# Kernel optimization log

Measured on AMD Instinct MI355X. Metric: run time of the kernel, lower is better.

The kernel has to match this reference:

```python
import jax, jax.numpy as jnp
import numpy as np
from jax import lax

B, T, I, H, O, L = 32, 1024, 128, 512, 128, 2


def _lstm_layer(x, Wih, Whh, bih, bhh):
    # x: [B, T, in]; Wih: [4H, in]; Whh: [4H, H]; PyTorch gate order i,f,g,o
    Hs = Whh.shape[1]
    # Precompute input contribution for all timesteps (one big GEMM)
    xg = jnp.einsum('bti,gi->btg', x, Wih) + bih + bhh  # [B, T, 4H]
    xg_t = jnp.swapaxes(xg, 0, 1)  # [T, B, 4H] for scan

    def step(carry, g_in):
        h, c = carry
        g = g_in + h @ Whh.T  # [B, 4H]
        i, f, gg, o = jnp.split(g, 4, axis=-1)
        i = jax.nn.sigmoid(i)
        f = jax.nn.sigmoid(f)
        gg = jnp.tanh(gg)
        o = jax.nn.sigmoid(o)
        c = f * c + i * gg
        h = o * jnp.tanh(c)
        return (h, c), h

    h0 = jnp.zeros((x.shape[0], Hs), dtype=x.dtype)
    c0 = jnp.zeros((x.shape[0], Hs), dtype=x.dtype)
    (_, _), hs = lax.scan(step, (h0, c0), xg_t)
    return jnp.swapaxes(hs, 0, 1)  # [B, T, H]


def setup_inputs() -> dict:
    key = jax.random.key(0)
    ks = jax.random.split(key, 16)
    s = 1.0 / np.sqrt(H)  # torch LSTM/Linear init scale
    u = lambda k, shape: jax.random.uniform(k, shape, jnp.float32, -s, s)
    return {
        'x': jax.random.normal(ks[0], (B, T, I), jnp.float32),
        'W_ih0': u(ks[1], (4 * H, I)), 'W_hh0': u(ks[2], (4 * H, H)),
        'b_ih0': u(ks[3], (4 * H,)), 'b_hh0': u(ks[4], (4 * H,)),
        'W_ih1': u(ks[5], (4 * H, H)), 'W_hh1': u(ks[6], (4 * H, H)),
        'b_ih1': u(ks[7], (4 * H,)), 'b_hh1': u(ks[8], (4 * H,)),
        'fcW': u(ks[9], (O, H)), 'fcb': u(ks[10], (O,)),
        'fc2W': jax.random.uniform(ks[11], (O, O), jnp.float32, -1.0 / np.sqrt(O), 1.0 / np.sqrt(O)),
        'fc2b': jax.random.uniform(ks[12], (O,), jnp.float32, -1.0 / np.sqrt(O), 1.0 / np.sqrt(O)),
    }


def reference(x, W_ih0, W_hh0, b_ih0, b_hh0, W_ih1, W_hh1, b_ih1, b_hh1, fcW, fcb, fc2W, fc2b):
    h1 = _lstm_layer(x, W_ih0, W_hh0, b_ih0, b_hh0)   # [B, T, H]
    h2 = _lstm_layer(h1, W_ih1, W_hh1, b_ih1, b_hh1)  # [B, T, H]
    out = h2 @ fcW.T + fcb    # [B, T, O]
    out2 = out @ fc2W.T + fc2b  # [B, T, O]
    return out2
```

## Files before the change

### kernel.cpp

```cpp
#include <hip/hip_runtime.h>
#include <math.h>

typedef _Float16 f16;
typedef _Float16 f16x8 __attribute__((ext_vector_type(8)));
typedef _Float16 f16x4 __attribute__((ext_vector_type(4)));
typedef _Float16 f16x2 __attribute__((ext_vector_type(2)));
typedef float f32x16 __attribute__((ext_vector_type(16)));
typedef int i32x4 __attribute__((ext_vector_type(4)));

#define B_ 32
#define T_ 1024
#define I_ 128
#define H_ 512

#define NWG 64
#define THR 512

#define OFF_FLAGS 0UL
#define OFF_H1S   4096UL
#define OFF_H2S   33591296UL
#define OFF_XT    67178496UL

__device__ inline f32x16 mfma32(f16x8 a, f16x8 b, f32x16 c) {
  return __builtin_amdgcn_mfma_f32_32x32x16_f16(a, b, c, 0, 0, 0);
}
__device__ inline float fast_sig(float x) { return 1.f / (1.f + __expf(-x)); }
__device__ inline float fast_tanh(float x) {
  float e = __expf(-2.f * fabsf(x));
  float t = (1.f - e) / (1.f + e);
  return x < 0.f ? -t : t;
}

__device__ inline unsigned ld_sc1_u32(const unsigned* p) {
  unsigned r;
  asm volatile("global_load_dword %0, %1, off sc1\n\ts_waitcnt vmcnt(0)"
               : "=v"(r) : "v"(p) : "memory");
  return r;
}
__device__ inline void st_sc1_u32(unsigned* p, unsigned v) {
  asm volatile("global_store_dword %0, %1, off sc1" :: "v"(p), "v"(v) : "memory");
}

__device__ inline int swz_h(int b, int kbyte) { return b * 1024 + (kbyte ^ ((b & 7) << 4)); }
__device__ inline int swz_x(int b, int kbyte) { return b * 256  + (kbyte ^ ((b & 7) << 4)); }

__global__ __launch_bounds__(256) void prep_xT(const float* __restrict__ x, f16* __restrict__ xT) {
  const int idx = blockIdx.x * 256 + threadIdx.x;
  const int n4 = B_ * T_ * I_ / 4;
  if (idx < n4) {
    const int i4 = idx * 4;
    const int i  = i4 & (I_ - 1);
    const int tt = (i4 >> 7) & (T_ - 1);
    const int b  = i4 >> 17;
    float4 v = *(const float4*)(x + i4);
    f16x4 o;
    o[0] = (f16)v.x; o[1] = (f16)v.y; o[2] = (f16)v.z; o[3] = (f16)v.w;
    *(f16x4*)(xT + ((size_t)tt * B_ + b) * I_ + i) = o;
  }
}

__global__ __launch_bounds__(THR, 1) void lstm_persist(
    const float* __restrict__ Wih0, const float* __restrict__ Whh0,
    const float* __restrict__ bih0, const float* __restrict__ bhh0,
    const float* __restrict__ Wih1, const float* __restrict__ Whh1,
    const float* __restrict__ bih1, const float* __restrict__ bhh1,
    char* ws) {
  __shared__ i32x4 h1l4[2048];
  __shared__ i32x4 h2l4[2048];
  __shared__ i32x4 xl4[512];
  __shared__ float gbuf[2 * 32 * 68];
  __shared__ float biasl[64];

  const int tid  = threadIdx.x;
  const int wgid = blockIdx.x;
  const int role = wgid >> 5;
  const int gid  = wgid & 31;
  const int lane = tid & 63;
  const int wv   = tid >> 6;
  const int nt   = wv & 1;
  const int kq   = (wv >> 1) & 1;
  const int bl   = lane & 31;
  const int kg   = lane >> 5;

  unsigned* flags0 = (unsigned*)(ws + OFF_FLAGS);
  unsigned* flags1 = (unsigned*)(ws + OFF_FLAGS + 2048);
  const char* h1base = ws + OFF_H1S;
  const char* h2base = ws + OFF_H2S;

  if (tid < 64) {
    const int g = tid >> 4, hc = tid & 15;
    const int row = g * 512 + gid * 16 + hc;
    biasl[tid] = role ? (bih1[row] + bhh1[row]) : (bih0[row] + bhh0[row]);
  }

  const int n    = nt * 32 + bl;
  const int wrow = (n >> 4) * 512 + gid * 16 + (n & 15);
  f16x8 wreg[32];
  if (role == 0) {
    if (wv < 4) {
#pragma unroll
      for (int ks = 0; ks < 20; ++ks) {
        const int k = kq * 320 + ks * 16 + kg * 8;
        const float* src = (k < I_) ? (Wih0 + (size_t)wrow * I_ + k)
                                    : (Whh0 + (size_t)wrow * H_ + (k - I_));
        float4 v0 = *(const float4*)(src);
        float4 v1 = *(const float4*)(src + 4);
        f16x8 h;
        h[0] = (f16)v0.x; h[1] = (f16)v0.y; h[2] = (f16)v0.z; h[3] = (f16)v0.w;
        h[4] = (f16)v1.x; h[5] = (f16)v1.y; h[6] = (f16)v1.z; h[7] = (f16)v1.w;
        wreg[ks] = h;
      }
    }
  } else {
    if (wv < 4) {
#pragma unroll
      for (int ks = 0; ks < 32; ++ks) {
        const int k = kq * 512 + ks * 16 + kg * 8;
        const float* src = (k < H_) ? (Wih1 + (size_t)wrow * H_ + k)
                                    : (Whh1 + (size_t)wrow * H_ + (k - H_));
        float4 v0 = *(const float4*)(src);
        float4 v1 = *(const float4*)(src + 4);
        f16x8 h;
        h[0] = (f16)v0.x; h[1] = (f16)v0.y; h[2] = (f16)v0.z; h[3] = (f16)v0.w;
        h[4] = (f16)v1.x; h[5] = (f16)v1.y; h[6] = (f16)v1.z; h[7] = (f16)v1.w;
        wreg[ks] = h;
      }
    }
  }

  float cst0 = 0.f, cst1 = 0.f;
  const char* h1c = (const char*)h1l4;
  const char* h2c = (const char*)h2l4;
  const char* xc  = (const char*)xl4;

  __syncthreads();

  if (role == 0) {
    for (int s = 0; s < T_; ++s) {
      i32x4 xv = ((const i32x4*)(ws + OFF_XT))[(size_t)s * 512 + tid];

      if (s >= 1) {
        if (tid < 64) {
          const unsigned tgt = (unsigned)s;
          const unsigned* fp = flags0 + (tid < 32 ? tid : 0) * 16;
          const bool active = tid < 32;
          for (;;) {
            unsigned v = ld_sc1_u32(fp);
            if (!active) v = tgt;
            if (__all((int)(v >= tgt))) break;
            __builtin_amdgcn_s_sleep(1);
          }
        }
        __syncthreads();
      }

      {
        const i32x4* src = (const i32x4*)(h1base + (size_t)s * 32768);
#pragma unroll
        for (int r = 0; r < 4; ++r) {
          const int u = r * 512 + tid;
          i32x4 v = src[u];
          const int wgs = u >> 6, b = (u >> 1) & 31, half = u & 1;
          *(i32x4*)((char*)h1l4 + swz_h(b, wgs * 32 + half * 16)) = v;
        }
      }
      *(i32x4*)((char*)xl4 + swz_x(tid >> 4, (tid & 15) * 16)) = xv;
      __syncthreads();

      if (wv < 4) {
        f32x16 acc = {};
        if (kq == 0) {
#pragma unroll
          for (int ks = 0; ks < 8; ++ks) {
            f16x8 a = *(const f16x8*)(xc + swz_x(bl, (ks * 16 + kg * 8) * 2));
            acc = mfma32(a, wreg[ks], acc);
          }
#pragma unroll
          for (int ks = 8; ks < 20; ++ks) {
            f16x8 a = *(const f16x8*)(h1c + swz_h(bl, (ks * 16 + kg * 8 - I_) * 2));
            acc = mfma32(a, wreg[ks], acc);
          }
        } else {
#pragma unroll
          for (int ks = 0; ks < 20; ++ks) {
            f16x8 a = *(const f16x8*)(h1c + swz_h(bl, (192 + ks * 16 + kg * 8) * 2));
            acc = mfma32(a, wreg[ks], acc);
          }
        }
        const int cb = nt * 32 + bl;
#pragma unroll
        for (int r = 0; r < 16; ++r) {
          const int row = (r & 3) + 8 * (r >> 2) + 4 * kg;
          gbuf[kq * 2176 + row * 68 + cb] = acc[r];
        }
      }
      __syncthreads();

      if (tid < 256) {
        const int rb = tid >> 3, hp = tid & 7;
        const float* gr = gbuf + rb * 68;
        float hv[2];
#pragma unroll
        for (int cc = 0; cc < 2; ++cc) {
          const int c = 2 * hp + cc;
          const float pi = gr[c]      + gr[2176 + c]      + biasl[c];
          const float pf = gr[16 + c] + gr[2176 + 16 + c] + biasl[16 + c];
          const float pg = gr[32 + c] + gr[2176 + 32 + c] + biasl[32 + c];
          const float po = gr[48 + c] + gr[2176 + 48 + c] + biasl[48 + c];
          const float ig = fast_sig(pi), fg = fast_sig(pf);
          const float gg = fast_tanh(pg), og = fast_sig(po);
          const float cprev = cc ? cst1 : cst0;
          const float cnew = fg * cprev + ig * gg;
          if (cc) cst1 = cnew; else cst0 = cnew;
          hv[cc] = og * fast_tanh(cnew);
        }
        f16x2 pk; pk[0] = (f16)hv[0]; pk[1] = (f16)hv[1];
        unsigned* dst = (unsigned*)(h1base + (size_t)(s + 1) * 32768 +
                                    (size_t)gid * 1024 + rb * 32 + hp * 4);
        st_sc1_u32(dst, __builtin_bit_cast(unsigned, pk));
      }

      asm volatile("s_waitcnt vmcnt(0)" ::: "memory");
      __syncthreads();
      if (tid == 0) st_sc1_u32(flags0 + gid * 16, (unsigned)(s + 1));
      __builtin_amdgcn_sched_barrier(0);
    }
  } else {
    for (int t = 0; t < T_; ++t) {
      if (tid < 64) {
        for (;;) {
          unsigned v, tgt;
          if (lane < 32) { v = ld_sc1_u32(flags0 + lane * 16); tgt = (unsigned)(t + 1); }
          else           { v = ld_sc1_u32(flags1 + (lane - 32) * 16); tgt = (unsigned)t; }
          if (__all((int)(v >= tgt))) break;
          __builtin_amdgcn_s_sleep(1);
        }
      }
      __syncthreads();

      {
        const i32x4* src = (const i32x4*)(h1base + (size_t)(t + 1) * 32768);
#pragma unroll
        for (int r = 0; r < 4; ++r) {
          const int u = r * 512 + tid;
          i32x4 v = src[u];
          const int wgs = u >> 6, b = (u >> 1) & 31, half = u & 1;
          *(i32x4*)((char*)h1l4 + swz_h(b, wgs * 32 + half * 16)) = v;
        }
      }
      {
        const i32x4* src = (const i32x4*)(h2base + (size_t)t * 32768);
#pragma unroll
        for (int r = 0; r < 4; ++r) {
          const int u = r * 512 + tid;
          i32x4 v = src[u];
          const int wgs = u >> 6, b = (u >> 1) & 31, half = u & 1;
          *(i32x4*)((char*)h2l4 + swz_h(b, wgs * 32 + half * 16)) = v;
        }
      }
      __syncthreads();

      if (wv < 4) {
        f32x16 acc = {};
        if (kq == 0) {
#pragma unroll
          for (int ks = 0; ks < 32; ++ks) {
            f16x8 a = *(const f16x8*)(h1c + swz_h(bl, (ks * 16 + kg * 8) * 2));
            acc = mfma32(a, wreg[ks], acc);
          }
        } else {
#pragma unroll
          for (int ks = 0; ks < 32; ++ks) {
            f16x8 a = *(const f16x8*)(h2c + swz_h(bl, (ks * 16 + kg * 8) * 2));
            acc = mfma32(a, wreg[ks], acc);
          }
        }
        const int cb = nt * 32 + bl;
#pragma unroll
        for (int r = 0; r < 16; ++r) {
          const int row = (r & 3) + 8 * (r >> 2) + 4 * kg;
          gbuf[kq * 2176 + row * 68 + cb] = acc[r];
        }
      }
      __syncthreads();

      if (tid < 256) {
        const int rb = tid >> 3, hp = tid & 7;
        const float* gr = gbuf + rb * 68;
        float hv[2];
#pragma unroll
        for (int cc = 0; cc < 2; ++cc) {
          const int c = 2 * hp + cc;
          const float pi = gr[c]      + gr[2176 + c]      + biasl[c];
          const float pf = gr[16 + c] + gr[2176 + 16 + c] + biasl[16 + c];
          const float pg = gr[32 + c] + gr[2176 + 32 + c] + biasl[32 + c];
          const float po = gr[48 + c] + gr[2176 + 48 + c] + biasl[48 + c];
          const float ig = fast_sig(pi), fg = fast_sig(pf);
          const float gg = fast_tanh(pg), og = fast_sig(po);
          const float cprev = cc ? cst1 : cst0;
          const float cnew = fg * cprev + ig * gg;
          if (cc) cst1 = cnew; else cst0 = cnew;
          hv[cc] = og * fast_tanh(cnew);
        }
        f16x2 pk; pk[0] = (f16)hv[0]; pk[1] = (f16)hv[1];
        unsigned* dst = (unsigned*)(h2base + (size_t)(t + 1) * 32768 +
                                    (size_t)gid * 1024 + rb * 32 + hp * 4);
        st_sc1_u32(dst, __builtin_bit_cast(unsigned, pk));
      }

      asm volatile("s_waitcnt vmcnt(0)" ::: "memory");
      __syncthreads();
      if (tid == 0) st_sc1_u32(flags1 + gid * 16, (unsigned)(t + 1));
      __builtin_amdgcn_sched_barrier(0);
    }
  }
}

__global__ __launch_bounds__(256) void fc_fused(const char* __restrict__ ws_h2,
                                                const float* __restrict__ fcW,
                                                const float* __restrict__ fcb,
                                                const float* __restrict__ fc2W,
                                                const float* __restrict__ fc2b,
                                                float* __restrict__ out) {
  __shared__ float hT[64][36];
  __shared__ float wT[128][36];
  __shared__ float oL[64][136];
  const int bt0 = blockIdx.x * 64;
  const int b   = bt0 >> 10;
  const int t0  = bt0 & 1023;
  const int t = threadIdx.x;
  const int c4 = (t & 31) * 4;
  const int rowg = t >> 5;
  float acc[8][4];
#pragma unroll
  for (int r = 0; r < 8; ++r)
#pragma unroll
    for (int j = 0; j < 4; ++j) acc[r][j] = 0.f;

  for (int kc = 0; kc < 16; ++kc) {
    {
      const int r = t >> 2, q = t & 3;
      const int c0 = kc * 32 + q * 8;
      const f16x8 v = *(const f16x8*)(ws_h2 + (size_t)(t0 + r + 1) * 32768 +
                                      (size_t)(c0 >> 4) * 1024 + b * 32 + (c0 & 15) * 2);
#pragma unroll
      for (int j = 0; j < 8; ++j) hT[r][q * 8 + j] = (float)v[j];
    }
#pragma unroll
    for (int u = t; u < 1024; u += 256) {
      const int cc = u >> 3, k4 = u & 7;
      *(float4*)&wT[cc][k4 * 4] = *(const float4*)(fcW + (size_t)cc * 512 + kc * 32 + k4 * 4);
    }
    __syncthreads();
#pragma unroll
    for (int k4 = 0; k4 < 8; ++k4) {
      float4 w0 = *(float4*)&wT[c4 + 0][k4 * 4];
      float4 w1 = *(float4*)&wT[c4 + 1][k4 * 4];
      float4 w2 = *(float4*)&wT[c4 + 2][k4 * 4];
      float4 w3 = *(float4*)&wT[c4 + 3][k4 * 4];
#pragma unroll
      for (int rr = 0; rr < 8; ++rr) {
        float4 h = *(float4*)&hT[rowg * 8 + rr][k4 * 4];
        acc[rr][0] += h.x * w0.x + h.y * w0.y + h.z * w0.z + h.w * w0.w;
        acc[rr][1] += h.x * w1.x + h.y * w1.y + h.z * w1.z + h.w * w1.w;
        acc[rr][2] += h.x * w2.x + h.y * w2.y + h.z * w2.z + h.w * w2.w;
        acc[rr][3] += h.x * w3.x + h.y * w3.y + h.z * w3.z + h.w * w3.w;
      }
    }
    __syncthreads();
  }
#pragma unroll
  for (int rr = 0; rr < 8; ++rr)
#pragma unroll
    for (int j = 0; j < 4; ++j)
      oL[rowg * 8 + rr][c4 + j] = acc[rr][j] + fcb[c4 + j];
  __syncthreads();
  float a2[8][4];
#pragma unroll
  for (int r = 0; r < 8; ++r)
#pragma unroll
    for (int j = 0; j < 4; ++j) a2[r][j] = 0.f;
#pragma unroll
  for (int k4 = 0; k4 < 32; ++k4) {
    float4 w0 = *(const float4*)(fc2W + (size_t)(c4 + 0) * 128 + k4 * 4);
    float4 w1 = *(const float4*)(fc2W + (size_t)(c4 + 1) * 128 + k4 * 4);
    float4 w2 = *(const float4*)(fc2W + (size_t)(c4 + 2) * 128 + k4 * 4);
    float4 w3 = *(const float4*)(fc2W + (size_t)(c4 + 3) * 128 + k4 * 4);
#pragma unroll
    for (int rr = 0; rr < 8; ++rr) {
      float4 h = *(float4*)&oL[rowg * 8 + rr][k4 * 4];
      a2[rr][0] += h.x * w0.x + h.y * w0.y + h.z * w0.z + h.w * w0.w;
      a2[rr][1] += h.x * w1.x + h.y * w1.y + h.z * w1.z + h.w * w1.w;
      a2[rr][2] += h.x * w2.x + h.y * w2.y + h.z * w2.z + h.w * w2.w;
      a2[rr][3] += h.x * w3.x + h.y * w3.y + h.z * w3.z + h.w * w3.w;
    }
  }
#pragma unroll
  for (int rr = 0; rr < 8; ++rr) {
    const int r = bt0 + rowg * 8 + rr;
#pragma unroll
    for (int j = 0; j < 4; ++j)
      out[(size_t)r * 128 + c4 + j] = a2[rr][j] + fc2b[c4 + j];
  }
}

extern "C" void kernel_launch(void* const* d_in, const int* in_sizes, int n_in,
                              void* d_out, int out_size, void* d_ws, size_t ws_size,
                              hipStream_t stream) {
  (void)in_sizes; (void)n_in; (void)out_size; (void)ws_size;
  const float* x    = (const float*)d_in[0];
  const float* Wih0 = (const float*)d_in[1];
  const float* Whh0 = (const float*)d_in[2];
  const float* bih0 = (const float*)d_in[3];
  const float* bhh0 = (const float*)d_in[4];
  const float* Wih1 = (const float*)d_in[5];
  const float* Whh1 = (const float*)d_in[6];
  const float* bih1 = (const float*)d_in[7];
  const float* bhh1 = (const float*)d_in[8];
  const float* fcW  = (const float*)d_in[9];
  const float* fcb  = (const float*)d_in[10];
  const float* fc2W = (const float*)d_in[11];
  const float* fc2b = (const float*)d_in[12];

  char* ws = (char*)d_ws;
  f16* xT = (f16*)(ws + OFF_XT);
  float* out = (float*)d_out;

  (void)hipMemsetAsync(ws + OFF_FLAGS, 0, 4096, stream);
  (void)hipMemsetAsync(ws + OFF_H1S, 0, 32768, stream);
  (void)hipMemsetAsync(ws + OFF_H2S, 0, 32768, stream);

  prep_xT<<<4096, 256, 0, stream>>>(x, xT);
  lstm_persist<<<NWG, THR, 0, stream>>>(Wih0, Whh0, bih0, bhh0,
                                        Wih1, Whh1, bih1, bhh1, ws);
  fc_fused<<<512, 256, 0, stream>>>(ws + OFF_H2S, fcW, fcb, fc2W, fc2b, out);
}
```

Measured before the change: 3.794 ms.

## Replace store-drain-and-flag sync with per-step checksum trailers for optimistic reads

Instead of waiting for all hidden-state stores to drain (s_waitcnt vmcnt(0) plus a barrier) before publishing a per-workgroup flag, each workgroup now writes a per-timestep trailer holding the epoch and two XOR checksums of the slice it produced. Consumers poll the trailer epoch, then load the data and trailer together and retry until the checksums match. This is meant to take the store-drain and one barrier off the critical path of the recurrent loop. In exchange it adds checksum computation, wave shuffles, extra loads and retry loops, and relies on checksum matching for consistency, giving up after 256 attempts.

```diff
diff --git a/kernel.cpp b/kernel.cpp
--- a/kernel.cpp
+++ b/kernel.cpp
@@ -16,10 +16,11 @@
 #define NWG 64
 #define THR 512
 
-#define OFF_FLAGS 0UL
-#define OFF_H1S   4096UL
-#define OFF_H2S   33591296UL
-#define OFF_XT    67178496UL
+#define OFF_TR1   0UL
+#define OFF_TR2   525312UL
+#define OFF_H1S   1050624UL
+#define OFF_H2S   34637824UL
+#define OFF_XT    68225024UL
 
 __device__ inline f32x16 mfma32(f16x8 a, f16x8 b, f32x16 c) {
   return __builtin_amdgcn_mfma_f32_32x32x16_f16(a, b, c, 0, 0, 0);
@@ -30,6 +31,9 @@
   float t = (1.f - e) / (1.f + e);
   return x < 0.f ? -t : t;
 }
+__device__ inline unsigned rotl32(unsigned d, unsigned r) {
+  return (d << r) | (d >> ((32u - r) & 31u));
+}
 
 __device__ inline unsigned ld_sc1_u32(const unsigned* p) {
   unsigned r;
@@ -39,6 +43,31 @@
 }
 __device__ inline void st_sc1_u32(unsigned* p, unsigned v) {
   asm volatile("global_store_dword %0, %1, off sc1" :: "v"(p), "v"(v) : "memory");
+}
+__device__ inline void st_sc1_b128(void* p, i32x4 v) {
+  asm volatile("global_store_dwordx4 %0, %1, off sc1" :: "v"(p), "v"(v) : "memory");
+}
+__device__ inline i32x4 ld_sc1_b128_async(const void* p) {
+  i32x4 r;
+  asm volatile("global_load_dwordx4 %0, %1, off sc1" : "=&v"(r) : "v"(p) : "memory");
+  return r;
+}
+__device__ inline void wait_vm0() {
+  asm volatile("s_waitcnt vmcnt(0)" ::: "memory");
+  __builtin_amdgcn_sched_barrier(0);
+}
+
+__device__ inline bool verify1(i32x4 d, i32x4 t, int lane, int epoch) {
+  unsigned p0 = (unsigned)d.x ^ (unsigned)d.y ^ (unsigned)d.z ^ (unsigned)d.w;
+  const unsigned base = (unsigned)(4 * lane) & 31u;
+  unsigned p1 = rotl32((unsigned)d.x, base) ^ rotl32((unsigned)d.y, base + 1) ^
+                rotl32((unsigned)d.z, base + 2) ^ rotl32((unsigned)d.w, base + 3);
+#pragma unroll
+  for (int m = 1; m < 64; m <<= 1) {
+    p0 ^= (unsigned)__shfl_xor((int)p0, m, 64);
+    p1 ^= (unsigned)__shfl_xor((int)p1, m, 64);
+  }
+  return ((unsigned)t.x == (unsigned)epoch) & ((unsigned)t.y == p0) & ((unsigned)t.z == p1);
 }
 
 __device__ inline int swz_h(int b, int kbyte) { return b * 1024 + (kbyte ^ ((b & 7) << 4)); }
@@ -70,6 +99,7 @@
   __shared__ i32x4 xl4[512];
   __shared__ float gbuf[2 * 32 * 68];
   __shared__ float biasl[64];
+  __shared__ unsigned cks[256];
 
   const int tid  = threadIdx.x;
   const int wgid = blockIdx.x;
@@ -82,8 +112,8 @@
   const int bl   = lane & 31;
   const int kg   = lane >> 5;
 
-  unsigned* flags0 = (unsigned*)(ws + OFF_FLAGS);
-  unsigned* flags1 = (unsigned*)(ws + OFF_FLAGS + 2048);
+  char* tr1 = ws + OFF_TR1;
+  char* tr2 = ws + OFF_TR2;
   const char* h1base = ws + OFF_H1S;
   const char* h2base = ws + OFF_H2S;
 
@@ -141,13 +171,10 @@
 
       if (s >= 1) {
         if (tid < 64) {
-          const unsigned tgt = (unsigned)s;
-          const unsigned* fp = flags0 + (tid < 32 ? tid : 0) * 16;
-          const bool active = tid < 32;
+          const unsigned* ep = (const unsigned*)(tr1 + (size_t)s * 512 + (lane & 31) * 16);
           for (;;) {
-            unsigned v = ld_sc1_u32(fp);
-            if (!active) v = tgt;
-            if (__all((int)(v >= tgt))) break;
+            unsigned v = (lane < 32) ? ld_sc1_u32(ep) : (unsigned)s;
+            if (__all((int)(v == (unsigned)s))) break;
             __builtin_amdgcn_s_sleep(1);
           }
         }
@@ -155,13 +182,42 @@
       }
 
       {
-        const i32x4* src = (const i32x4*)(h1base + (size_t)s * 32768);
+        const char* src = h1base + (size_t)s * 32768;
+        const char* trs = tr1 + (size_t)s * 512;
+        i32x4 d1[4], t1[4];
+#pragma unroll
+        for (int r = 0; r < 4; ++r) d1[r] = ld_sc1_b128_async(src + (r * 512 + tid) * 16);
+        if (s >= 1) {
+#pragma unroll
+          for (int r = 0; r < 4; ++r) t1[r] = ld_sc1_b128_async(trs + (r * 8 + wv) * 16);
+        }
+        wait_vm0();
+        if (s >= 1) {
+          bool ok0 = verify1(d1[0], t1[0], lane, s), ok1 = verify1(d1[1], t1[1], lane, s);
+          bool ok2 = verify1(d1[2], t1[2], lane, s), ok3 = verify1(d1[3], t1[3], lane, s);
+          int att = 0;
+          while (!(ok0 && ok1 && ok2 && ok3)) {
+            if (++att > 256) break;
+            if (!ok0) { d1[0] = ld_sc1_b128_async(src + (0 * 512 + tid) * 16);
+                        t1[0] = ld_sc1_b128_async(trs + (0 * 8 + wv) * 16); }
+            if (!ok1) { d1[1] = ld_sc1_b128_async(src + (1 * 512 + tid) * 16);
+                        t1[1] = ld_sc1_b128_async(trs + (1 * 8 + wv) * 16); }
+            if (!ok2) { d1[2] = ld_sc1_b128_async(src + (2 * 512 + tid) * 16);
+                        t1[2] = ld_sc1_b128_async(trs + (2 * 8 + wv) * 16); }
+            if (!ok3) { d1[3] = ld_sc1_b128_async(src + (3 * 512 + tid) * 16);
+                        t1[3] = ld_sc1_b128_async(trs + (3 * 8 + wv) * 16); }
+            wait_vm0();
+            if (!ok0) ok0 = verify1(d1[0], t1[0], lane, s);
+            if (!ok1) ok1 = verify1(d1[1], t1[1], lane, s);
+            if (!ok2) ok2 = verify1(d1[2], t1[2], lane, s);
+            if (!ok3) ok3 = verify1(d1[3], t1[3], lane, s);
+          }
+        }
 #pragma unroll
         for (int r = 0; r < 4; ++r) {
           const int u = r * 512 + tid;
-          i32x4 v = src[u];
           const int wgs = u >> 6, b = (u >> 1) & 31, half = u & 1;
-          *(i32x4*)((char*)h1l4 + swz_h(b, wgs * 32 + half * 16)) = v;
+          *(i32x4*)((char*)h1l4 + swz_h(b, wgs * 32 + half * 16)) = d1[r];
         }
       }
       *(i32x4*)((char*)xl4 + swz_x(tid >> 4, (tid & 15) * 16)) = xv;
@@ -215,47 +271,104 @@
           hv[cc] = og * fast_tanh(cnew);
         }
         f16x2 pk; pk[0] = (f16)hv[0]; pk[1] = (f16)hv[1];
-        unsigned* dst = (unsigned*)(h1base + (size_t)(s + 1) * 32768 +
-                                    (size_t)gid * 1024 + rb * 32 + hp * 4);
-        st_sc1_u32(dst, __builtin_bit_cast(unsigned, pk));
-      }
-
-      asm volatile("s_waitcnt vmcnt(0)" ::: "memory");
-      __syncthreads();
-      if (tid == 0) st_sc1_u32(flags0 + gid * 16, (unsigned)(s + 1));
+        const unsigned dw = __builtin_bit_cast(unsigned, pk);
+        st_sc1_u32((unsigned*)(h1base + (size_t)(s + 1) * 32768 +
+                               (size_t)gid * 1024 + rb * 32 + hp * 4), dw);
+        cks[tid] = dw;
+      }
+      __syncthreads();
+
+      if (wv == 0) {
+        unsigned q0 = cks[lane] ^ cks[64 + lane] ^ cks[128 + lane] ^ cks[192 + lane];
+        unsigned q1 = rotl32(q0, (unsigned)lane & 31u);
+#pragma unroll
+        for (int m = 1; m < 64; m <<= 1) {
+          q0 ^= (unsigned)__shfl_xor((int)q0, m, 64);
+          q1 ^= (unsigned)__shfl_xor((int)q1, m, 64);
+        }
+        if (lane == 0) {
+          i32x4 tr; tr.x = s + 1; tr.y = (int)q0; tr.z = (int)q1; tr.w = 0;
+          st_sc1_b128(tr1 + (size_t)(s + 1) * 512 + gid * 16, tr);
+        }
+      }
       __builtin_amdgcn_sched_barrier(0);
     }
   } else {
     for (int t = 0; t < T_; ++t) {
       if (tid < 64) {
+        const unsigned* ep1 = (const unsigned*)(tr1 + (size_t)(t + 1) * 512 + (lane & 31) * 16);
+        const unsigned* ep2 = (const unsigned*)(tr2 + (size_t)t * 512 + (lane & 31) * 16);
         for (;;) {
           unsigned v, tgt;
-          if (lane < 32) { v = ld_sc1_u32(flags0 + lane * 16); tgt = (unsigned)(t + 1); }
-          else           { v = ld_sc1_u32(flags1 + (lane - 32) * 16); tgt = (unsigned)t; }
-          if (__all((int)(v >= tgt))) break;
+          if (lane < 32)      { v = ld_sc1_u32(ep1); tgt = (unsigned)(t + 1); }
+          else if (t >= 1)    { v = ld_sc1_u32(ep2); tgt = (unsigned)t; }
+          else                { v = 0; tgt = 0; }
+          if (__all((int)(v == tgt))) break;
           __builtin_amdgcn_s_sleep(1);
         }
       }
       __syncthreads();
 
       {
-        const i32x4* src = (const i32x4*)(h1base + (size_t)(t + 1) * 32768);
+        const char* s1 = h1base + (size_t)(t + 1) * 32768;
+        const char* r1 = tr1 + (size_t)(t + 1) * 512;
+        const char* s2 = h2base + (size_t)t * 32768;
+        const char* r2 = tr2 + (size_t)t * 512;
+        i32x4 d1[4], t1[4], d2[4], t2[4];
+#pragma unroll
+        for (int r = 0; r < 4; ++r) {
+          d1[r] = ld_sc1_b128_async(s1 + (r * 512 + tid) * 16);
+          d2[r] = ld_sc1_b128_async(s2 + (r * 512 + tid) * 16);
+          t1[r] = ld_sc1_b128_async(r1 + (r * 8 + wv) * 16);
+        }
+        if (t >= 1) {
+#pragma unroll
+          for (int r = 0; r < 4; ++r) t2[r] = ld_sc1_b128_async(r2 + (r * 8 + wv) * 16);
+        }
+        wait_vm0();
+        {
+          bool a0 = verify1(d1[0], t1[0], lane, t + 1), a1 = verify1(d1[1], t1[1], lane, t + 1);
+          bool a2 = verify1(d1[2], t1[2], lane, t + 1), a3 = verify1(d1[3], t1[3], lane, t + 1);
+          bool b0 = (t < 1) || verify1(d2[0], t2[0], lane, t);
+          bool b1 = (t < 1) || verify1(d2[1], t2[1], lane, t);
+          bool b2 = (t < 1) || verify1(d2[2], t2[2], lane, t);
+          bool b3 = (t < 1) || verify1(d2[3], t2[3], lane, t);
+          int att = 0;
+          while (!(a0 && a1 && a2 && a3 && b0 && b1 && b2 && b3)) {
+            if (++att > 256) break;
+            if (!a0) { d1[0] = ld_sc1_b128_async(s1 + (0 * 512 + tid) * 16);
+                       t1[0] = ld_sc1_b128_async(r1 + (0 * 8 + wv) * 16); }
+            if (!a1) { d1[1] = ld_sc1_b128_async(s1 + (1 * 512 + tid) * 16);
+                       t1[1] = ld_sc1_b128_async(r1 + (1 * 8 + wv) * 16); }
+            if (!a2) { d1[2] = ld_sc1_b128_async(s1 + (2 * 512 + tid) * 16);
+                       t1[2] = ld_sc1_b128_async(r1 + (2 * 8 + wv) * 16); }
+            if (!a3) { d1[3] = ld_sc1_b128_async(s1 + (3 * 512 + tid) * 16);
+                       t1[3] = ld_sc1_b128_async(r1 + (3 * 8 + wv) * 16); }
+            if (!b0) { d2[0] = ld_sc1_b128_async(s2 + (0 * 512 + tid) * 16);
+                       t2[0] = ld_sc1_b128_async(r2 + (0 * 8 + wv) * 16); }
+            if (!b1) { d2[1] = ld_sc1_b128_async(s2 + (1 * 512 + tid) * 16);
+                       t2[1] = ld_sc1_b128_async(r2 + (1 * 8 + wv) * 16); }
+            if (!b2) { d2[2] = ld_sc1_b128_async(s2 + (2 * 512 + tid) * 16);
+                       t2[2] = ld_sc1_b128_async(r2 + (2 * 8 + wv) * 16); }
+            if (!b3) { d2[3] = ld_sc1_b128_async(s2 + (3 * 512 + tid) * 16);
+                       t2[3] = ld_sc1_b128_async(r2 + (3 * 8 + wv) * 16); }
+            wait_vm0();
+            if (!a0) a0 = verify1(d1[0], t1[0], lane, t + 1);
+            if (!a1) a1 = verify1(d1[1], t1[1], lane, t + 1);
+            if (!a2) a2 = verify1(d1[2], t1[2], lane, t + 1);
+            if (!a3) a3 = verify1(d1[3], t1[3], lane, t + 1);
+            if (!b0) b0 = verify1(d2[0], t2[0], lane, t);
+            if (!b1) b1 = verify1(d2[1], t2[1], lane, t);
+            if (!b2) b2 = verify1(d2[2], t2[2], lane, t);
+            if (!b3) b3 = verify1(d2[3], t2[3], lane, t);
+          }
+        }
 #pragma unroll
         for (int r = 0; r < 4; ++r) {
           const int u = r * 512 + tid;
-          i32x4 v = src[u];
           const int wgs = u >> 6, b = (u >> 1) & 31, half = u & 1;
-          *(i32x4*)((char*)h1l4 + swz_h(b, wgs * 32 + half * 16)) = v;
-        }
-      }
-      {
-        const i32x4* src = (const i32x4*)(h2base + (size_t)t * 32768);
-#pragma unroll
-        for (int r = 0; r < 4; ++r) {
-          const int u = r * 512 + tid;
-          i32x4 v = src[u];
-          const int wgs = u >> 6, b = (u >> 1) & 31, half = u & 1;
-          *(i32x4*)((char*)h2l4 + swz_h(b, wgs * 32 + half * 16)) = v;
+          *(i32x4*)((char*)h1l4 + swz_h(b, wgs * 32 + half * 16)) = d1[r];
+          *(i32x4*)((char*)h2l4 + swz_h(b, wgs * 32 + half * 16)) = d2[r];
         }
       }
       __syncthreads();
@@ -303,14 +416,26 @@
           hv[cc] = og * fast_tanh(cnew);
         }
         f16x2 pk; pk[0] = (f16)hv[0]; pk[1] = (f16)hv[1];
-        unsigned* dst = (unsigned*)(h2base + (size_t)(t + 1) * 32768 +
-                                    (size_t)gid * 1024 + rb * 32 + hp * 4);
-        st_sc1_u32(dst, __builtin_bit_cast(unsigned, pk));
-      }
-
-      asm volatile("s_waitcnt vmcnt(0)" ::: "memory");
-      __syncthreads();
-      if (tid == 0) st_sc1_u32(flags1 + gid * 16, (unsigned)(t + 1));
+        const unsigned dw = __builtin_bit_cast(unsigned, pk);
+        st_sc1_u32((unsigned*)(h2base + (size_t)(t + 1) * 32768 +
+                               (size_t)gid * 1024 + rb * 32 + hp * 4), dw);
+        cks[tid] = dw;
+      }
+      __syncthreads();
+
+      if (wv == 0) {
+        unsigned q0 = cks[lane] ^ cks[64 + lane] ^ cks[128 + lane] ^ cks[192 + lane];
+        unsigned q1 = rotl32(q0, (unsigned)lane & 31u);
+#pragma unroll
+        for (int m = 1; m < 64; m <<= 1) {
+          q0 ^= (unsigned)__shfl_xor((int)q0, m, 64);
+          q1 ^= (unsigned)__shfl_xor((int)q1, m, 64);
+        }
+        if (lane == 0) {
+          i32x4 tr; tr.x = t + 1; tr.y = (int)q0; tr.z = (int)q1; tr.w = 0;
+          st_sc1_b128(tr2 + (size_t)(t + 1) * 512 + gid * 16, tr);
+        }
+      }
       __builtin_amdgcn_sched_barrier(0);
     }
   }
@@ -426,7 +551,6 @@
   f16* xT = (f16*)(ws + OFF_XT);
   float* out = (float*)d_out;
 
-  (void)hipMemsetAsync(ws + OFF_FLAGS, 0, 4096, stream);
   (void)hipMemsetAsync(ws + OFF_H1S, 0, 32768, stream);
   (void)hipMemsetAsync(ws + OFF_H2S, 0, 32768, stream);
 
```

After: 8.062 ms. 112% more time.
